# Kernel tuning notes

Hardware: AMD Instinct MI355X
Metric: run time of the kernel (lower is better)

## Reference

```python
import jax, jax.numpy as jnp
import numpy as np

N, E, C, D_E, G = 50000, 800000, 64, 32, 512


def setup_inputs() -> dict:
    key = jax.random.key(0)
    ks = jax.random.split(key, 12)
    inp = {
        "x": jax.random.normal(ks[0], (N, C), dtype=jnp.float32),
        "edge_index": jax.random.randint(ks[1], (2, E), 0, N, dtype=jnp.int64),
        "edge_attr": jax.random.normal(ks[2], (E, D_E), dtype=jnp.float32),
        "batch": jnp.sort(jax.random.randint(ks[3], (N,), 0, G, dtype=jnp.int64)),
        "num_graphs": G,
        # CGConv gating linears: Linear(2*C + D_E, C)
        "W_f": jax.random.normal(ks[4], (2 * C + D_E, C), dtype=jnp.float32) * 0.05,
        "b_f": jnp.zeros((C,), dtype=jnp.float32),
        "W_s": jax.random.normal(ks[5], (2 * C + D_E, C), dtype=jnp.float32) * 0.05,
        "b_s": jnp.zeros((C,), dtype=jnp.float32),
        # head MLP
        "W1": jax.random.normal(ks[6], (C, 6), dtype=jnp.float32) * 0.1,
        "b1": jnp.zeros((6,), dtype=jnp.float32),
        "W2": jax.random.normal(ks[7], (6, 1), dtype=jnp.float32) * 0.1,
        "b2": jnp.zeros((1,), dtype=jnp.float32),
    }
    return inp


def cg_conv(x, edge_index, edge_attr, W_f, b_f, W_s, b_s):
    src, dst = edge_index[0], edge_index[1]
    # PyG CGConv message: z = cat([x_i (dst), x_j (src), edge_attr])
    z = jnp.concatenate([x[dst], x[src], edge_attr], axis=-1)  # [E, 2C+D]
    msg = jax.nn.sigmoid(z @ W_f + b_f) * jax.nn.softplus(z @ W_s + b_s)  # [E, C]
    agg = jax.ops.segment_sum(msg, dst, num_segments=x.shape[0])  # scatter-add to dst
    return x + agg  # residual


def reference(x, edge_index, edge_attr, batch, num_graphs, W_f, b_f, W_s, b_s, W1, b1, W2, b2):
    h = cg_conv(x, edge_index, edge_attr, W_f, b_f, W_s, b_s)  # [N, C]
    h = jax.nn.sigmoid(h)
    h = jax.nn.sigmoid(h @ W1 + b1)  # [N, 6]
    g = jax.ops.segment_sum(h, batch, num_segments=num_graphs)  # global_add_pool [G, 6]
    out = jax.nn.relu(g @ W2 + b2)  # [G, 1]
    return out
```

## Files before the change

kernel.cpp:

```cpp
#include <hip/hip_runtime.h>
#include <hip/hip_bf16.h>
#include <stdint.h>

#define NN 50000
#define EE 800000
#define CC 64
#define DE 32
#define KD 160
#define NC 128
#define GG 512
#define SCAN_B 1024
#define NSCAN ((NN + SCAN_B - 1) / SCAN_B)

typedef __attribute__((ext_vector_type(8))) short bf16x8;
typedef __attribute__((ext_vector_type(4))) float f32x4;

__device__ __forceinline__ float sigmoidf_(float v) {
  return __fdividef(1.f, 1.f + __expf(-v));
}
__device__ __forceinline__ float softplusf_(float v) {
  return fmaxf(v, 0.f) + __logf(1.f + __expf(-fabsf(v)));
}
__device__ __forceinline__ unsigned short f2bf(float f) {
  uint32_t u = __float_as_uint(f);
  return (unsigned short)((u + 0x7FFFu + ((u >> 16) & 1u)) >> 16);
}
__device__ __forceinline__ float bf2f(unsigned short h) {
  return __uint_as_float(((uint32_t)h) << 16);
}
__device__ __forceinline__ void tsplit(float f, short& hi, short& lo) {
  uint32_t u = __float_as_uint(f);
  float lf = f - __uint_as_float(u & 0xFFFF0000u);
  hi = (short)(u >> 16);
  lo = (short)(__float_as_uint(lf) >> 16);
}

__global__ void count_kernel(const int* __restrict__ ei, int* __restrict__ deg) {
  int e = blockIdx.x * 256 + threadIdx.x;
  atomicAdd(&deg[ei[EE + e]], 1);
}

__global__ __launch_bounds__(SCAN_B) void scan1_kernel(
    const int* __restrict__ deg, int* __restrict__ pos, int* __restrict__ bsum) {
  __shared__ int s[SCAN_B];
  int t = threadIdx.x, i = blockIdx.x * SCAN_B + t;
  s[t] = (i < NN) ? deg[i] : 0;
  __syncthreads();
  for (int off = 1; off < SCAN_B; off <<= 1) {
    int a = (t >= off) ? s[t - off] : 0;
    __syncthreads();
    s[t] += a;
    __syncthreads();
  }
  if (i < NN) pos[i + 1] = s[t];
  if (t == SCAN_B - 1) bsum[blockIdx.x] = s[t];
}

__global__ void scan2_kernel(int* __restrict__ bsum) {
  __shared__ int s[64];
  int t = threadIdx.x;
  s[t] = (t < NSCAN) ? bsum[t] : 0;
  __syncthreads();
  for (int off = 1; off < 64; off <<= 1) {
    int a = (t >= off) ? s[t - off] : 0;
    __syncthreads();
    s[t] += a;
    __syncthreads();
  }
  bsum[t] = (t == 0) ? 0 : s[t - 1];
}

__global__ __launch_bounds__(SCAN_B) void scan3_kernel(
    int* __restrict__ pos, const int* __restrict__ bsum, int* __restrict__ cursor) {
  int t = threadIdx.x, i = blockIdx.x * SCAN_B + t;
  if (i < NN) {
    int v = pos[i + 1] + bsum[blockIdx.x];
    pos[i + 1] = v;
    if (i + 1 < NN) cursor[i + 1] = v;
  }
  if (i == 0) { pos[0] = 0; cursor[0] = 0; }
}

__global__ void fill_kernel(const int* __restrict__ ei,
                            int* __restrict__ cursor, int* __restrict__ eidx) {
  int e = blockIdx.x * 256 + threadIdx.x;
  int d = ei[EE + e];
  int slot = atomicAdd(&cursor[d], 1);
  eidx[slot] = e;
}

__global__ void xsplit_kernel(const float* __restrict__ x,
                              unsigned short* __restrict__ xhi,
                              unsigned short* __restrict__ xlo) {
  int idx = blockIdx.x * 256 + threadIdx.x;
  float4 v = ((const float4*)x)[idx];
  ushort4 h, l;
  short a, b;
  tsplit(v.x, a, b); h.x = (unsigned short)a; l.x = (unsigned short)b;
  tsplit(v.y, a, b); h.y = (unsigned short)a; l.y = (unsigned short)b;
  tsplit(v.z, a, b); h.z = (unsigned short)a; l.z = (unsigned short)b;
  tsplit(v.w, a, b); h.w = (unsigned short)a; l.w = (unsigned short)b;
  *(ushort4*)(xhi + (size_t)idx * 4) = h;
  *(ushort4*)(xlo + (size_t)idx * 4) = l;
}

__global__ void wprep_kernel(const float* __restrict__ Wf, const float* __restrict__ Ws,
                             short* __restrict__ Bph, short* __restrict__ Bpl) {
  int p = blockIdx.x * 256 + threadIdx.x;
  int i = p & 7, l = (p >> 3) & 63, tile = p >> 9;
  int nt = tile & 7, s = tile >> 3;
  int k = s * 32 + 8 * (l >> 4) + i;
  int col = nt * 16 + (l & 15);
  float w = (col < CC) ? Wf[k * CC + col] : Ws[k * CC + (col - CC)];
  short hi, lo;
  tsplit(w, hi, lo);
  Bph[p] = hi;
  Bpl[p] = lo;
}

template <bool BF16MSG>
__global__ __launch_bounds__(512) void edge_mfma_kernel(
    const unsigned short* __restrict__ xhi, const unsigned short* __restrict__ xlo,
    const int* __restrict__ ei, const float* __restrict__ ea,
    const short* __restrict__ Bph, const short* __restrict__ Bpl,
    const float* __restrict__ bfv, const float* __restrict__ bsv,
    void* __restrict__ msg)
{
  __shared__ short Bh[20480];
  __shared__ short Bl[20480];
  const int t = threadIdx.x;

  {
    const float4* gh = (const float4*)Bph;
    const float4* gl = (const float4*)Bpl;
    float4* sh = (float4*)Bh;
    float4* sl = (float4*)Bl;
    #pragma unroll
    for (int r = 0; r < 5; ++r) {
      sh[r * 512 + t] = gh[r * 512 + t];
      sl[r * 512 + t] = gl[r * 512 + t];
    }
  }

  const int w  = t >> 6, l = t & 63;
  const int mg = w >> 1, ng = w & 1;
  const int ebase = blockIdx.x * 256 + mg * 64;
  const int lr = l & 15, lg = l >> 4;

  int e[4], dst[4], src[4];
  #pragma unroll
  for (int mt = 0; mt < 4; ++mt) {
    e[mt]   = ebase + mt * 16 + lr;
    dst[mt] = ei[EE + e[mt]];
    src[mt] = ei[e[mt]];
  }
  __syncthreads();

  f32x4 acc[4][4];
  #pragma unroll
  for (int mt = 0; mt < 4; ++mt)
    #pragma unroll
    for (int q = 0; q < 4; ++q) acc[mt][q] = (f32x4){0.f, 0.f, 0.f, 0.f};

  #pragma unroll
  for (int s = 0; s < 5; ++s) {
    bf16x8 ah[4], al[4];
    if (s < 4) {
      const int koff = (s & 1) * 32 + 8 * lg;
      #pragma unroll
      for (int mt = 0; mt < 4; ++mt) {
        const int row = (s < 2) ? dst[mt] : src[mt];
        const size_t o = (size_t)row * CC + koff;
        ah[mt] = *(const bf16x8*)(xhi + o);
        al[mt] = *(const bf16x8*)(xlo + o);
      }
    } else {
      #pragma unroll
      for (int mt = 0; mt < 4; ++mt) {
        const float4* p4 = (const float4*)(ea + (size_t)e[mt] * DE + 8 * lg);
        float4 v0 = p4[0], v1 = p4[1];
        float v[8] = {v0.x, v0.y, v0.z, v0.w, v1.x, v1.y, v1.z, v1.w};
        #pragma unroll
        for (int i = 0; i < 8; ++i) {
          short hh, ll;
          tsplit(v[i], hh, ll);
          ah[mt][i] = hh;
          al[mt][i] = ll;
        }
      }
    }
    bf16x8 bh[4], bl[4];
    #pragma unroll
    for (int q = 0; q < 4; ++q) {
      const int nt  = 2 * ng + (q & 1) + (q >> 1) * 4;
      const int off = ((s * 8 + nt) * 64 + l) * 8;
      bh[q] = *(const bf16x8*)(Bh + off);
      bl[q] = *(const bf16x8*)(Bl + off);
    }
    #pragma unroll
    for (int mt = 0; mt < 4; ++mt)
      #pragma unroll
      for (int q = 0; q < 4; ++q)
        acc[mt][q] = __builtin_amdgcn_mfma_f32_16x16x32_bf16(ah[mt], bh[q], acc[mt][q], 0, 0, 0);
    #pragma unroll
    for (int mt = 0; mt < 4; ++mt)
      #pragma unroll
      for (int q = 0; q < 4; ++q)
        acc[mt][q] = __builtin_amdgcn_mfma_f32_16x16x32_bf16(al[mt], bh[q], acc[mt][q], 0, 0, 0);
    #pragma unroll
    for (int mt = 0; mt < 4; ++mt)
      #pragma unroll
      for (int q = 0; q < 4; ++q)
        acc[mt][q] = __builtin_amdgcn_mfma_f32_16x16x32_bf16(ah[mt], bl[q], acc[mt][q], 0, 0, 0);
  }

  #pragma unroll
  for (int p2 = 0; p2 < 2; ++p2) {
    const int ch = (2 * ng + p2) * 16 + lr;
    const float bF = bfv[ch], bS = bsv[ch];
    #pragma unroll
    for (int mt = 0; mt < 4; ++mt) {
      f32x4 F = acc[mt][p2];
      f32x4 S = acc[mt][p2 + 2];
      #pragma unroll
      for (int r = 0; r < 4; ++r) {
        const int edge = ebase + mt * 16 + lg * 4 + r;
        const float mval = sigmoidf_(F[r] + bF) * softplusf_(S[r] + bS);
        if constexpr (!BF16MSG) {
          ((float*)msg)[(size_t)edge * CC + ch] = mval;
        } else {
          ((unsigned short*)msg)[(size_t)edge * CC + ch] = f2bf(mval);
        }
      }
    }
  }
}

template <bool BF16MSG>
__global__ __launch_bounds__(256) void gather_node_kernel(
    const void* __restrict__ msg, const int* __restrict__ pos,
    const int* __restrict__ eidx, const float* __restrict__ x,
    const int* __restrict__ batch,
    const float* __restrict__ W1, const float* __restrict__ b1,
    float* __restrict__ pool)
{
  const int t = threadIdx.x;
  const int n = blockIdx.x * 16 + (t >> 4);
  const int i = t & 15;
  const int start = pos[n], end = pos[n + 1];

  float4 acc = make_float4(0.f, 0.f, 0.f, 0.f);
  if constexpr (!BF16MSG) {
    const float4* m4 = (const float4*)msg;
    for (int p = start; p < end; ++p) {
      int e = eidx[p];
      float4 m = m4[(size_t)e * 16 + i];
      acc.x += m.x; acc.y += m.y; acc.z += m.z; acc.w += m.w;
    }
  } else {
    const unsigned short* mb = (const unsigned short*)msg;
    for (int p = start; p < end; ++p) {
      int e = eidx[p];
      ushort4 u = *(const ushort4*)(mb + (size_t)e * CC + 4 * i);
      acc.x += bf2f(u.x); acc.y += bf2f(u.y); acc.z += bf2f(u.z); acc.w += bf2f(u.w);
    }
  }

  const float4 xv = *(const float4*)(x + (size_t)n * CC + 4 * i);
  float h0 = sigmoidf_(xv.x + acc.x);
  float h1 = sigmoidf_(xv.y + acc.y);
  float h2 = sigmoidf_(xv.z + acc.z);
  float h3 = sigmoidf_(xv.w + acc.w);

  float o[6];
  const float* wp = W1 + (size_t)(4 * i) * 6;
  #pragma unroll
  for (int j = 0; j < 6; ++j) {
    o[j] = h0 * wp[j] + h1 * wp[6 + j] + h2 * wp[12 + j] + h3 * wp[18 + j];
  }
  #pragma unroll
  for (int d = 8; d > 0; d >>= 1) {
    #pragma unroll
    for (int j = 0; j < 6; ++j) o[j] += __shfl_down(o[j], d, 16);
  }
  if (i == 0) {
    int g = batch[n];
    #pragma unroll
    for (int j = 0; j < 6; ++j)
      atomicAdd(&pool[g * 6 + j], sigmoidf_(o[j] + b1[j]));
  }
}

__global__ void out_kernel(const float* __restrict__ pool,
                           const float* __restrict__ W2,
                           const float* __restrict__ b2,
                           float* __restrict__ out)
{
  int g = blockIdx.x * 64 + threadIdx.x;
  if (g < GG) {
    float acc = b2[0];
    #pragma unroll
    for (int j = 0; j < 6; ++j) acc = fmaf(pool[g * 6 + j], W2[j], acc);
    out[g] = fmaxf(acc, 0.f);
  }
}

static inline size_t al64(size_t v) { return (v + 63) & ~(size_t)63; }

extern "C" void kernel_launch(void* const* d_in, const int* in_sizes, int n_in,
                              void* d_out, int out_size, void* d_ws, size_t ws_size,
                              hipStream_t stream) {
  const float* x     = (const float*)d_in[0];
  const int*   ei    = (const int*)d_in[1];
  const float* ea    = (const float*)d_in[2];
  const int*   batch = (const int*)d_in[3];
  const float* Wf = (const float*)d_in[5];
  const float* bf = (const float*)d_in[6];
  const float* Ws = (const float*)d_in[7];
  const float* bs = (const float*)d_in[8];
  const float* W1 = (const float*)d_in[9];
  const float* b1 = (const float*)d_in[10];
  const float* W2 = (const float*)d_in[11];
  const float* b2 = (const float*)d_in[12];
  float* out = (float*)d_out;

  const size_t fixed = al64((size_t)NN * CC * 2) * 2 +
                       al64((size_t)KD * NC * 2) * 2 +
                       al64((size_t)NN * 4) + al64((size_t)(NN + 1) * 4) +
                       al64((size_t)NN * 4) + al64(64 * 4) +
                       al64((size_t)EE * 4) + al64((size_t)GG * 6 * 4);
  const bool f32 = ws_size >= al64((size_t)EE * CC * 4) + fixed;

  char* p = (char*)d_ws;
  void* msg = (void*)p;
  p += al64(f32 ? (size_t)EE * CC * 4 : (size_t)EE * CC * 2);
  unsigned short* xhi = (unsigned short*)p; p += al64((size_t)NN * CC * 2);
  unsigned short* xlo = (unsigned short*)p; p += al64((size_t)NN * CC * 2);
  short* Bph = (short*)p; p += al64((size_t)KD * NC * 2);
  short* Bpl = (short*)p; p += al64((size_t)KD * NC * 2);
  int* deg    = (int*)p; p += al64((size_t)NN * 4);
  int* pos    = (int*)p; p += al64((size_t)(NN + 1) * 4);
  int* cursor = (int*)p; p += al64((size_t)NN * 4);
  int* bsum   = (int*)p; p += al64(64 * 4);
  int* eidx   = (int*)p; p += al64((size_t)EE * 4);
  float* pool = (float*)p;

  hipMemsetAsync(deg, 0, (size_t)NN * 4, stream);
  hipMemsetAsync(pool, 0, (size_t)GG * 6 * 4, stream);

  xsplit_kernel<<<NN * CC / 4 / 256, 256, 0, stream>>>(x, xhi, xlo);
  wprep_kernel<<<KD * NC / 256, 256, 0, stream>>>(Wf, Ws, Bph, Bpl);

  count_kernel<<<EE / 256, 256, 0, stream>>>(ei, deg);
  scan1_kernel<<<NSCAN, SCAN_B, 0, stream>>>(deg, pos, bsum);
  scan2_kernel<<<1, 64, 0, stream>>>(bsum);
  scan3_kernel<<<NSCAN, SCAN_B, 0, stream>>>(pos, bsum, cursor);
  fill_kernel<<<EE / 256, 256, 0, stream>>>(ei, cursor, eidx);

  if (f32) {
    edge_mfma_kernel<false><<<EE / 256, 512, 0, stream>>>(xhi, xlo, ei, ea, Bph, Bpl, bf, bs, msg);
    gather_node_kernel<false><<<NN / 16, 256, 0, stream>>>(msg, pos, eidx, x, batch, W1, b1, pool);
  } else {
    edge_mfma_kernel<true><<<EE / 256, 512, 0, stream>>>(xhi, xlo, ei, ea, Bph, Bpl, bf, bs, msg);
    gather_node_kernel<true><<<NN / 16, 256, 0, stream>>>(msg, pos, eidx, x, batch, W1, b1, pool);
  }
  out_kernel<<<(GG + 63) / 64, 64, 0, stream>>>(pool, W2, b2, out);
}
```

Before: 594.9 us.

## Process edges in CSR order so gather reads messages contiguously

The fill kernel now also records dst and src per sorted slot. The edge kernel processes edges in dst-sorted order and writes each message at its CSR slot, so the node gather reads contiguous rows with no eidx indirection. The x[dst] gathers in the edge kernel also become highly local. Separately, the low-part weight tile is read from global memory instead of LDS, halving shared-memory use to raise occupancy. The costs are extra fill writes and a scattered edge_attr read via eidx.

```diff
diff --git a/kernel.cpp b/kernel.cpp
--- a/kernel.cpp
+++ b/kernel.cpp
@@ -81,12 +81,16 @@
   if (i == 0) { pos[0] = 0; cursor[0] = 0; }
 }
 
-__global__ void fill_kernel(const int* __restrict__ ei,
-                            int* __restrict__ cursor, int* __restrict__ eidx) {
+__global__ void fill_kernel(const int* __restrict__ ei, int* __restrict__ cursor,
+                            int* __restrict__ eidx, int* __restrict__ dsts,
+                            int* __restrict__ srcs) {
   int e = blockIdx.x * 256 + threadIdx.x;
   int d = ei[EE + e];
+  int s = ei[e];
   int slot = atomicAdd(&cursor[d], 1);
   eidx[slot] = e;
+  dsts[slot] = d;
+  srcs[slot] = s;
 }
 
 __global__ void xsplit_kernel(const float* __restrict__ x,
@@ -121,38 +125,34 @@
 template <bool BF16MSG>
 __global__ __launch_bounds__(512) void edge_mfma_kernel(
     const unsigned short* __restrict__ xhi, const unsigned short* __restrict__ xlo,
-    const int* __restrict__ ei, const float* __restrict__ ea,
+    const int* __restrict__ eidx, const int* __restrict__ dsts,
+    const int* __restrict__ srcs, const float* __restrict__ ea,
     const short* __restrict__ Bph, const short* __restrict__ Bpl,
     const float* __restrict__ bfv, const float* __restrict__ bsv,
     void* __restrict__ msg)
 {
   __shared__ short Bh[20480];
-  __shared__ short Bl[20480];
   const int t = threadIdx.x;
 
   {
     const float4* gh = (const float4*)Bph;
-    const float4* gl = (const float4*)Bpl;
     float4* sh = (float4*)Bh;
-    float4* sl = (float4*)Bl;
-    #pragma unroll
-    for (int r = 0; r < 5; ++r) {
-      sh[r * 512 + t] = gh[r * 512 + t];
-      sl[r * 512 + t] = gl[r * 512 + t];
-    }
+    #pragma unroll
+    for (int r = 0; r < 5; ++r) sh[r * 512 + t] = gh[r * 512 + t];
   }
 
   const int w  = t >> 6, l = t & 63;
   const int mg = w >> 1, ng = w & 1;
-  const int ebase = blockIdx.x * 256 + mg * 64;
+  const int sbase = blockIdx.x * 256 + mg * 64;
   const int lr = l & 15, lg = l >> 4;
 
-  int e[4], dst[4], src[4];
+  int dst[4], src[4], ep[4];
   #pragma unroll
   for (int mt = 0; mt < 4; ++mt) {
-    e[mt]   = ebase + mt * 16 + lr;
-    dst[mt] = ei[EE + e[mt]];
-    src[mt] = ei[e[mt]];
+    const int slot = sbase + mt * 16 + lr;
+    dst[mt] = dsts[slot];
+    src[mt] = srcs[slot];
+    ep[mt]  = eidx[slot];
   }
   __syncthreads();
 
@@ -161,6 +161,8 @@
   for (int mt = 0; mt < 4; ++mt)
     #pragma unroll
     for (int q = 0; q < 4; ++q) acc[mt][q] = (f32x4){0.f, 0.f, 0.f, 0.f};
+
+  const bf16x8* Blg = (const bf16x8*)Bpl;
 
   #pragma unroll
   for (int s = 0; s < 5; ++s) {
@@ -177,7 +179,7 @@
     } else {
       #pragma unroll
       for (int mt = 0; mt < 4; ++mt) {
-        const float4* p4 = (const float4*)(ea + (size_t)e[mt] * DE + 8 * lg);
+        const float4* p4 = (const float4*)(ea + (size_t)ep[mt] * DE + 8 * lg);
         float4 v0 = p4[0], v1 = p4[1];
         float v[8] = {v0.x, v0.y, v0.z, v0.w, v1.x, v1.y, v1.z, v1.w};
         #pragma unroll
@@ -193,9 +195,8 @@
     #pragma unroll
     for (int q = 0; q < 4; ++q) {
       const int nt  = 2 * ng + (q & 1) + (q >> 1) * 4;
-      const int off = ((s * 8 + nt) * 64 + l) * 8;
-      bh[q] = *(const bf16x8*)(Bh + off);
-      bl[q] = *(const bf16x8*)(Bl + off);
+      bh[q] = *(const bf16x8*)(Bh + ((s * 8 + nt) * 64 + l) * 8);
+      bl[q] = Blg[(s * 8 + nt) * 64 + l];
     }
     #pragma unroll
     for (int mt = 0; mt < 4; ++mt)
@@ -224,12 +225,12 @@
       f32x4 S = acc[mt][p2 + 2];
       #pragma unroll
       for (int r = 0; r < 4; ++r) {
-        const int edge = ebase + mt * 16 + lg * 4 + r;
+        const int oslot = sbase + mt * 16 + lg * 4 + r;
         const float mval = sigmoidf_(F[r] + bF) * softplusf_(S[r] + bS);
         if constexpr (!BF16MSG) {
-          ((float*)msg)[(size_t)edge * CC + ch] = mval;
+          ((float*)msg)[(size_t)oslot * CC + ch] = mval;
         } else {
-          ((unsigned short*)msg)[(size_t)edge * CC + ch] = f2bf(mval);
+          ((unsigned short*)msg)[(size_t)oslot * CC + ch] = f2bf(mval);
         }
       }
     }
@@ -239,8 +240,7 @@
 template <bool BF16MSG>
 __global__ __launch_bounds__(256) void gather_node_kernel(
     const void* __restrict__ msg, const int* __restrict__ pos,
-    const int* __restrict__ eidx, const float* __restrict__ x,
-    const int* __restrict__ batch,
+    const float* __restrict__ x, const int* __restrict__ batch,
     const float* __restrict__ W1, const float* __restrict__ b1,
     float* __restrict__ pool)
 {
@@ -253,15 +253,13 @@
   if constexpr (!BF16MSG) {
     const float4* m4 = (const float4*)msg;
     for (int p = start; p < end; ++p) {
-      int e = eidx[p];
-      float4 m = m4[(size_t)e * 16 + i];
+      float4 m = m4[(size_t)p * 16 + i];
       acc.x += m.x; acc.y += m.y; acc.z += m.z; acc.w += m.w;
     }
   } else {
     const unsigned short* mb = (const unsigned short*)msg;
     for (int p = start; p < end; ++p) {
-      int e = eidx[p];
-      ushort4 u = *(const ushort4*)(mb + (size_t)e * CC + 4 * i);
+      ushort4 u = *(const ushort4*)(mb + (size_t)p * CC + 4 * i);
       acc.x += bf2f(u.x); acc.y += bf2f(u.y); acc.z += bf2f(u.z); acc.w += bf2f(u.w);
     }
   }
@@ -328,7 +326,8 @@
                        al64((size_t)KD * NC * 2) * 2 +
                        al64((size_t)NN * 4) + al64((size_t)(NN + 1) * 4) +
                        al64((size_t)NN * 4) + al64(64 * 4) +
-                       al64((size_t)EE * 4) + al64((size_t)GG * 6 * 4);
+                       al64((size_t)EE * 4) * 3 +
+                       al64((size_t)GG * 6 * 4);
   const bool f32 = ws_size >= al64((size_t)EE * CC * 4) + fixed;
 
   char* p = (char*)d_ws;
@@ -343,6 +342,8 @@
   int* cursor = (int*)p; p += al64((size_t)NN * 4);
   int* bsum   = (int*)p; p += al64(64 * 4);
   int* eidx   = (int*)p; p += al64((size_t)EE * 4);
+  int* dsts   = (int*)p; p += al64((size_t)EE * 4);
+  int* srcs   = (int*)p; p += al64((size_t)EE * 4);
   float* pool = (float*)p;
 
   hipMemsetAsync(deg, 0, (size_t)NN * 4, stream);
@@ -355,14 +356,14 @@
   scan1_kernel<<<NSCAN, SCAN_B, 0, stream>>>(deg, pos, bsum);
   scan2_kernel<<<1, 64, 0, stream>>>(bsum);
   scan3_kernel<<<NSCAN, SCAN_B, 0, stream>>>(pos, bsum, cursor);
-  fill_kernel<<<EE / 256, 256, 0, stream>>>(ei, cursor, eidx);
+  fill_kernel<<<EE / 256, 256, 0, stream>>>(ei, cursor, eidx, dsts, srcs);
 
   if (f32) {
-    edge_mfma_kernel<false><<<EE / 256, 512, 0, stream>>>(xhi, xlo, ei, ea, Bph, Bpl, bf, bs, msg);
-    gather_node_kernel<false><<<NN / 16, 256, 0, stream>>>(msg, pos, eidx, x, batch, W1, b1, pool);
+    edge_mfma_kernel<false><<<EE / 256, 512, 0, stream>>>(xhi, xlo, eidx, dsts, srcs, ea, Bph, Bpl, bf, bs, msg);
+    gather_node_kernel<false><<<NN / 16, 256, 0, stream>>>(msg, pos, x, batch, W1, b1, pool);
   } else {
-    edge_mfma_kernel<true><<<EE / 256, 512, 0, stream>>>(xhi, xlo, ei, ea, Bph, Bpl, bf, bs, msg);
-    gather_node_kernel<true><<<NN / 16, 256, 0, stream>>>(msg, pos, eidx, x, batch, W1, b1, pool);
+    edge_mfma_kernel<true><<<EE / 256, 512, 0, stream>>>(xhi, xlo, eidx, dsts, srcs, ea, Bph, Bpl, bf, bs, msg);
+    gather_node_kernel<true><<<NN / 16, 256, 0, stream>>>(msg, pos, x, batch, W1, b1, pool);
   }
   out_kernel<<<(GG + 63) / 64, 64, 0, stream>>>(pool, W2, b2, out);
 }
```

Result: faster. 561.2 us (-5.7%).
